# Optimization experiments

Hardware: AMD Instinct MI355X
Metric: run time of the kernel (lower is better)

Reference implementation:

```python
import jax, jax.numpy as jnp
import numpy as np

N_NODES = 100000
N_EDGES = 1600000
N_CLASS = 26
HIDDEN = 128


def gcn_conv(x, W, b, row, col, ew, n):
    """PyG GCNConv with normalize=True, add_self_loops=True (fill 1.0).

    row/col/ew already include self-loops. x: [N, Fin], W: [Fin, Fout].
    """
    deg = jax.ops.segment_sum(ew, col, num_segments=n)            # [N]
    dis = jnp.where(deg > 0, jax.lax.rsqrt(jnp.maximum(deg, 1e-30)), 0.0)
    norm = dis[row] * ew * dis[col]                               # [E+N]
    h = x @ W                                                     # [N, Fout]
    msg = h[row] * norm[:, None]                                  # gather + scale
    out = jax.ops.segment_sum(msg, col, num_segments=n)           # scatter-add
    return out + b


def setup_inputs() -> dict:
    key = jax.random.key(0)
    k1, k2, k3, k4, k5, k6, k7, k8, k9 = jax.random.split(key, 9)
    x = jax.random.normal(k1, (N_NODES, N_CLASS), dtype=jnp.float32)
    edge_index = jax.random.randint(k2, (2, N_EDGES), 0, N_NODES, dtype=jnp.int64)
    edge_weight = jax.random.uniform(k3, (N_EDGES,), dtype=jnp.float32)
    s1 = 1.0 / np.sqrt(N_CLASS)
    s2 = 1.0 / np.sqrt(HIDDEN)
    W1 = jax.random.uniform(k4, (N_CLASS, HIDDEN), jnp.float32, -s1, s1)
    b1 = jnp.zeros((HIDDEN,), jnp.float32)
    W2 = jax.random.uniform(k5, (HIDDEN, HIDDEN), jnp.float32, -s2, s2)
    b2 = jnp.zeros((HIDDEN,), jnp.float32)
    Wfc = jax.random.uniform(k6, (HIDDEN, N_CLASS), jnp.float32, -s2, s2)
    bfc = jax.random.uniform(k7, (N_CLASS,), jnp.float32, -s2, s2)
    return {"x": x, "edge_index": edge_index, "edge_weight": edge_weight,
            "W1": W1, "b1": b1, "W2": W2, "b2": b2, "Wfc": Wfc, "bfc": bfc}


def reference(x, edge_index, edge_weight, W1, b1, W2, b2, Wfc, bfc):
    n = x.shape[0]
    loop = jnp.arange(n, dtype=edge_index.dtype)
    row = jnp.concatenate([edge_index[0], loop])   # sources (with self-loops)
    col = jnp.concatenate([edge_index[1], loop])   # targets
    ew = jnp.concatenate([edge_weight, jnp.ones((n,), edge_weight.dtype)])
    h = jax.nn.relu(gcn_conv(x, W1, b1, row, col, ew, n))
    h = jax.nn.relu(gcn_conv(h, W2, b2, row, col, ew, n))
    return h @ Wfc + bfc
```

## Files before the change

### kernel.cpp

```cpp
#include <hip/hip_runtime.h>
#include <hip/hip_fp16.h>

#define N_NODES 100000
#define N_EDGES 1600000
#define HIDDEN  128
#define N_CLASS 26

#define BUK_SHIFT 9
#define BUK_DSTS  512
#define NBUK      196
#define BUK_CAP   10240
#define PB_EDGES  8192
#define PB_BLOCKS ((N_EDGES + PB_EDGES - 1) / PB_EDGES)

typedef _Float16 f16x2 __attribute__((ext_vector_type(2)));

__device__ __forceinline__ float fdot2(__half2 a, __half2 b, float c) {
#if __has_builtin(__builtin_amdgcn_fdot2)
    union { __half2 h; f16x2 v; } ua, ub;
    ua.h = a; ub.h = b;
    return __builtin_amdgcn_fdot2(ua.v, ub.v, c, false);
#else
    float2 fa = __half22float2(a), fb = __half22float2(b);
    return c + fa.x * fb.x + fa.y * fb.y;
#endif
}

union U4 { uint4 u; __half2 h[4]; };
union U2 { uint2 u; __half2 h[2]; };
union UW { int i; __half2 h; };


__global__ __launch_bounds__(1024) void bucket_kernel(const int* __restrict__ row,
                                                      const int* __restrict__ col,
                                                      const float* __restrict__ ew,
                                                      int* __restrict__ bukcnt,
                                                      int2* __restrict__ stage) {
    __shared__ int2 outst[PB_EDGES];
    __shared__ unsigned short bukof[PB_EDGES];
    __shared__ int cnt[NBUK], ofs[NBUK], cur[NBUK], gt[NBUK];
    __shared__ int sc[256];
    const int tid = threadIdx.x;
    const int e0 = blockIdx.x * PB_EDGES;
    const int nvalid = min(PB_EDGES, N_EDGES - e0);

    for (int b = tid; b < NBUK; b += 1024) { cnt[b] = 0; cur[b] = 0; }
    __syncthreads();

    int mykey[8]; float myw[8]; int mybuk[8];
#pragma unroll
    for (int i = 0; i < 8; ++i) {
        int idx = tid + i * 1024;
        mybuk[i] = -1;
        if (idx < nvalid) {
            int e = e0 + idx;
            int d = col[e], r = row[e];
            int buk = d >> BUK_SHIFT;
            mykey[i] = ((d & (BUK_DSTS - 1)) << 17) | r;
            myw[i] = ew[e];
            mybuk[i] = buk;
            atomicAdd(&cnt[buk], 1);
        }
    }
    __syncthreads();

    {
        int c = (tid < NBUK) ? cnt[tid] : 0;
        if (tid < 256) sc[tid] = c;
        __syncthreads();
        for (int o = 1; o < 256; o <<= 1) {
            int v = 0;
            if (tid < 256 && tid >= o) v = sc[tid - o];
            __syncthreads();
            if (tid < 256) sc[tid] += v;
            __syncthreads();
        }
        if (tid < NBUK) ofs[tid] = sc[tid] - c;
        __syncthreads();
    }

#pragma unroll
    for (int i = 0; i < 8; ++i) {
        if (mybuk[i] >= 0) {
            int s = ofs[mybuk[i]] + atomicAdd(&cur[mybuk[i]], 1);
            outst[s] = make_int2(mykey[i], __float_as_int(myw[i]));
            bukof[s] = (unsigned short)mybuk[i];
        }
    }
    __syncthreads();

    if (tid < NBUK) {
        int c = cnt[tid];
        int gb = (c > 0) ? atomicAdd(&bukcnt[tid], c) : 0;
        gt[tid] = tid * BUK_CAP + gb;
    }
    __syncthreads();

    for (int i = tid; i < nvalid; i += 1024) {
        int b = bukof[i];
        stage[(size_t)gt[b] + (i - ofs[b])] = outst[i];
    }
}


__global__ void bukscan_kernel(const int* __restrict__ bukcnt, int* __restrict__ bukbase,
                               int* __restrict__ start) {
    __shared__ int s[256];
    int tid = threadIdx.x;
    int c = (tid < NBUK) ? bukcnt[tid] : 0;
    s[tid] = c;
    __syncthreads();
    for (int o = 1; o < 256; o <<= 1) {
        int v = (tid >= o) ? s[tid - o] : 0;
        __syncthreads();
        s[tid] += v;
        __syncthreads();
    }
    if (tid < NBUK) bukbase[tid] = s[tid] - c;
    if (tid == 0) start[N_NODES] = N_EDGES;
}


__global__ __launch_bounds__(1024) void csr_kernel(const int2* __restrict__ stage,
                                                   const int* __restrict__ bukcnt,
                                                   const int* __restrict__ bukbase,
                                                   const float* __restrict__ x,
                                                   int* __restrict__ start,
                                                   float* __restrict__ dinv,
                                                   __half* __restrict__ x16,
                                                   int2* __restrict__ packed,
                                                   int* __restrict__ perm) {
    __shared__ unsigned int cnt5[BUK_DSTS];
    __shared__ int ofs5[BUK_DSTS];
    __shared__ unsigned int cur5[BUK_DSTS];
    __shared__ float deg5[BUK_DSTS];
    __shared__ float dv5[BUK_DSTS];
    __shared__ int sc[BUK_DSTS];
    __shared__ int dhist[128];
    __shared__ int dcur[128];
    const int tid = threadIdx.x;
    const int b = blockIdx.x;
    const int total = bukcnt[b];
    const int base = bukbase[b];
    const int2* st = stage + (size_t)b * BUK_CAP;

    for (int j = tid; j < BUK_DSTS; j += 1024) { cnt5[j] = 0; cur5[j] = 0; deg5[j] = 0.0f; }
    if (tid < 128) { dhist[tid] = 0; dcur[tid] = 0; }
    __syncthreads();

    for (int i = tid; i < total; i += 1024) {
        int2 en = st[i];
        int dl = en.x >> 17;
        atomicAdd(&cnt5[dl], 1u);
        atomicAdd(&deg5[dl], __int_as_float(en.y));
    }
    __syncthreads();

    {
        int c = (tid < BUK_DSTS) ? (int)cnt5[tid] : 0;
        if (tid < BUK_DSTS) sc[tid] = c;
        __syncthreads();
        for (int o = 1; o < BUK_DSTS; o <<= 1) {
            int v = 0;
            if (tid < BUK_DSTS && tid >= o) v = sc[tid - o];
            __syncthreads();
            if (tid < BUK_DSTS) sc[tid] += v;
            __syncthreads();
        }
        if (tid < BUK_DSTS) ofs5[tid] = sc[tid] - c;
        __syncthreads();
    }

    int myd = -1;
    {
        int d = (b << BUK_SHIFT) + tid;
        if (tid < BUK_DSTS && d < N_NODES) {
            myd = min((int)cnt5[tid], 127);
            atomicAdd(&dhist[myd], 1);
        }
    }

    if (tid < BUK_DSTS) {
        int d = (b << BUK_SHIFT) + tid;
        if (d < N_NODES) {
            float dv = rsqrtf(deg5[tid] + 1.0f);
            dv5[tid] = dv;
            dinv[d] = dv;
            start[d] = base + ofs5[tid];
        }
    }
    __syncthreads();

    if (tid < 128) sc[tid] = dhist[tid];
    __syncthreads();
    for (int o = 1; o < 128; o <<= 1) {
        int v = 0;
        if (tid < 128 && tid >= o) v = sc[tid - o];
        __syncthreads();
        if (tid < 128) sc[tid] += v;
        __syncthreads();
    }
    if (myd >= 0) {
        int rank = sc[myd] - dhist[myd] + atomicAdd(&dcur[myd], 1);
        perm[(b << BUK_SHIFT) + rank] = (b << BUK_SHIFT) + tid;
    }

    for (int t = tid; t < BUK_DSTS * 32; t += 1024) {
        int j = t >> 5, l = t & 31;
        int d = (b << BUK_SHIFT) + j;
        if (d < N_NODES) {
            float v = (l < N_CLASS) ? x[(size_t)d * N_CLASS + l] * dv5[j] : 0.0f;
            x16[((size_t)d << 5) + l] = __float2half(v);
        }
    }

    for (int i = tid; i < total; i += 1024) {
        int2 en = st[i];
        int dl = en.x >> 17;
        int src = en.x & 0x1FFFF;
        unsigned int r = atomicAdd(&cur5[dl], 1u);
        unsigned int hw = __half_as_ushort(__float2half(__int_as_float(en.y)));
        packed[(size_t)base + ofs5[dl] + (int)r] = make_int2(src, (int)(hw | (hw << 16)));
    }
}


__global__ __launch_bounds__(256) void layer1_kernel(const __half* __restrict__ x16,
                                                     const int* __restrict__ start,
                                                     const int2* __restrict__ packed,
                                                     const float* __restrict__ dinv,
                                                     const int* __restrict__ perm,
                                                     const float* __restrict__ W1,
                                                     const float* __restrict__ b1,
                                                     __half* __restrict__ h16) {
    __shared__ float axs[32][32];
    __shared__ int gl[32];
    const int tid = threadIdx.x;
    const int nb = blockIdx.x * 32;
    {
        const int j = tid >> 3;
        const int l = tid & 7;
        const int g = perm[nb + j];
        if (l == 0) gl[j] = g;
        const uint2* X = reinterpret_cast<const uint2*>(x16);
        U2 sv; sv.u = X[((size_t)g << 3) + l];
        __half2 acc0 = sv.h[0], acc1 = sv.h[1];
        int s = start[g], t = start[g + 1];
        int i = s;
        for (; i + 4 <= t; i += 4) {
            int2 p0 = packed[i], p1 = packed[i + 1], p2 = packed[i + 2], p3 = packed[i + 3];
            U2 v0, v1, v2, v3;
            v0.u = X[((size_t)p0.x << 3) + l];
            v1.u = X[((size_t)p1.x << 3) + l];
            v2.u = X[((size_t)p2.x << 3) + l];
            v3.u = X[((size_t)p3.x << 3) + l];
            UW w0, w1, w2, w3;
            w0.i = p0.y; w1.i = p1.y; w2.i = p2.y; w3.i = p3.y;
            acc0 = __hfma2(w0.h, v0.h[0], acc0); acc1 = __hfma2(w0.h, v0.h[1], acc1);
            acc0 = __hfma2(w1.h, v1.h[0], acc0); acc1 = __hfma2(w1.h, v1.h[1], acc1);
            acc0 = __hfma2(w2.h, v2.h[0], acc0); acc1 = __hfma2(w2.h, v2.h[1], acc1);
            acc0 = __hfma2(w3.h, v3.h[0], acc0); acc1 = __hfma2(w3.h, v3.h[1], acc1);
        }
        for (; i < t; ++i) {
            int2 p = packed[i];
            U2 v; v.u = X[((size_t)p.x << 3) + l];
            UW w; w.i = p.y;
            acc0 = __hfma2(w.h, v.h[0], acc0); acc1 = __hfma2(w.h, v.h[1], acc1);
        }
        float dg = dinv[g];
        float2 a = __half22float2(acc0), bb = __half22float2(acc1);
        *reinterpret_cast<float4*>(&axs[j][l * 4]) =
            make_float4(dg * a.x, dg * a.y, dg * bb.x, dg * bb.y);
    }
    __syncthreads();
    const int c = tid & 127;
    const int half = tid >> 7;
    float w[N_CLASS];
#pragma unroll
    for (int k = 0; k < N_CLASS; ++k) w[k] = W1[k * HIDDEN + c];
    const float bias = b1[c];
#pragma unroll
    for (int tt = 0; tt < 16; ++tt) {
        int n = half + 2 * tt;
        float acc = bias;
#pragma unroll
        for (int k = 0; k < N_CLASS; ++k) acc += axs[n][k] * w[k];
        h16[(size_t)gl[n] * HIDDEN + c] = __float2half(fmaxf(acc, 0.0f));
    }
}


#define CB_NODES 128
__global__ __launch_bounds__(512) void gemmC_kernel(const __half* __restrict__ h16,
                                                    const float* __restrict__ W2,
                                                    const float* __restrict__ dinv,
                                                    __half* __restrict__ p16) {
    __shared__ __half2 hs2[CB_NODES][HIDDEN / 2];
    __shared__ __half2 ws2[HIDDEN / 2][HIDDEN];
    const int tid = threadIdx.x;
    const int nb = blockIdx.x * CB_NODES;
    for (int t = tid; t < HIDDEN / 2 * HIDDEN; t += 512) {
        int k2 = t >> 7, c = t & 127;
        ws2[k2][c] = __floats2half2_rn(W2[(2 * k2) * HIDDEN + c], W2[(2 * k2 + 1) * HIDDEN + c]);
    }
    for (int t = tid; t < CB_NODES * 16; t += 512) {
        int node = nb + (t >> 4);
        reinterpret_cast<uint4*>(hs2)[t] =
            (node < N_NODES)
                ? reinterpret_cast<const uint4*>(h16)[(size_t)node * 16 + (t & 15)]
                : make_uint4(0u, 0u, 0u, 0u);
    }
    __syncthreads();
    const int c4 = (tid & 31) * 4;
    const int n0 = (tid >> 5) * 8;
    float acc[8][4] = {};
    for (int k2 = 0; k2 < HIDDEN / 2; k2 += 2) {
        U4 wa, wb;
        wa.u = *reinterpret_cast<const uint4*>(&ws2[k2][c4]);
        wb.u = *reinterpret_cast<const uint4*>(&ws2[k2 + 1][c4]);
#pragma unroll
        for (int i = 0; i < 8; ++i) {
            U2 hv; hv.u = *reinterpret_cast<const uint2*>(&hs2[n0 + i][k2]);
#pragma unroll
            for (int q = 0; q < 4; ++q) {
                acc[i][q] = fdot2(hv.h[0], wa.h[q], acc[i][q]);
                acc[i][q] = fdot2(hv.h[1], wb.h[q], acc[i][q]);
            }
        }
    }
#pragma unroll
    for (int i = 0; i < 8; ++i) {
        int node = nb + n0 + i;
        if (node < N_NODES) {
            float d = dinv[node];
            union { __half2 h2[2]; uint2 u; } pk;
            pk.h2[0] = __floats2half2_rn(d * acc[i][0], d * acc[i][1]);
            pk.h2[1] = __floats2half2_rn(d * acc[i][2], d * acc[i][3]);
            *reinterpret_cast<uint2*>(&p16[(size_t)node * HIDDEN + c4]) = pk.u;
        }
    }
}


__global__ __launch_bounds__(256) void aggfc_kernel(const __half* __restrict__ p16,
                                                    const int* __restrict__ start,
                                                    const int2* __restrict__ packed,
                                                    const float* __restrict__ dinv,
                                                    const int* __restrict__ perm,
                                                    const float* __restrict__ b2,
                                                    const float* __restrict__ Wfc,
                                                    const float* __restrict__ bfc,
                                                    float* __restrict__ out) {
    __shared__ __half2 wf2[HIDDEN / 2][N_CLASS];
    __shared__ float bfs[N_CLASS];
    __shared__ __half2 zs2[16][65];
    const int tid = threadIdx.x;
    for (int t = tid; t < HIDDEN / 2 * N_CLASS; t += 256) {
        int k2 = t / N_CLASS, j = t % N_CLASS;
        wf2[k2][j] = __floats2half2_rn(Wfc[(2 * k2) * N_CLASS + j], Wfc[(2 * k2 + 1) * N_CLASS + j]);
    }
    if (tid < N_CLASS) bfs[tid] = bfc[tid];
    __syncthreads();

    const int grp = tid >> 4;
    const int l   = tid & 15;
    const int g   = perm[blockIdx.x * 16 + grp];
    const uint4* P = reinterpret_cast<const uint4*>(p16);

    U4 sv; sv.u = P[((size_t)g << 4) + l];
    __half2 acc0 = sv.h[0], acc1 = sv.h[1], acc2 = sv.h[2], acc3 = sv.h[3];

    int s = start[g], t = start[g + 1];
    int i = s;
    for (; i + 4 <= t; i += 4) {
        int2 pa = packed[i], pb = packed[i + 1], pc = packed[i + 2], pd = packed[i + 3];
        U4 va, vb, vc, vd;
        va.u = P[((size_t)pa.x << 4) + l];
        vb.u = P[((size_t)pb.x << 4) + l];
        vc.u = P[((size_t)pc.x << 4) + l];
        vd.u = P[((size_t)pd.x << 4) + l];
        UW wa, wb, wc, wd; wa.i = pa.y; wb.i = pb.y; wc.i = pc.y; wd.i = pd.y;
        acc0 = __hfma2(wa.h, va.h[0], acc0); acc1 = __hfma2(wa.h, va.h[1], acc1);
        acc2 = __hfma2(wa.h, va.h[2], acc2); acc3 = __hfma2(wa.h, va.h[3], acc3);
        acc0 = __hfma2(wb.h, vb.h[0], acc0); acc1 = __hfma2(wb.h, vb.h[1], acc1);
        acc2 = __hfma2(wb.h, vb.h[2], acc2); acc3 = __hfma2(wb.h, vb.h[3], acc3);
        acc0 = __hfma2(wc.h, vc.h[0], acc0); acc1 = __hfma2(wc.h, vc.h[1], acc1);
        acc2 = __hfma2(wc.h, vc.h[2], acc2); acc3 = __hfma2(wc.h, vc.h[3], acc3);
        acc0 = __hfma2(wd.h, vd.h[0], acc0); acc1 = __hfma2(wd.h, vd.h[1], acc1);
        acc2 = __hfma2(wd.h, vd.h[2], acc2); acc3 = __hfma2(wd.h, vd.h[3], acc3);
    }
    for (; i < t; ++i) {
        int2 p = packed[i];
        U4 v; v.u = P[((size_t)p.x << 4) + l];
        UW w; w.i = p.y;
        acc0 = __hfma2(w.h, v.h[0], acc0); acc1 = __hfma2(w.h, v.h[1], acc1);
        acc2 = __hfma2(w.h, v.h[2], acc2); acc3 = __hfma2(w.h, v.h[3], acc3);
    }

    const float dg = dinv[g];
    const int f = l * 8;
    float4 ba = *reinterpret_cast<const float4*>(&b2[f]);
    float4 bb = *reinterpret_cast<const float4*>(&b2[f + 4]);
    float2 f0 = __half22float2(acc0), f1 = __half22float2(acc1);
    float2 f2 = __half22float2(acc2), f3 = __half22float2(acc3);
    zs2[grp][l * 4 + 0] = __floats2half2_rn(fmaxf(dg * f0.x + ba.x, 0.f), fmaxf(dg * f0.y + ba.y, 0.f));
    zs2[grp][l * 4 + 1] = __floats2half2_rn(fmaxf(dg * f1.x + ba.z, 0.f), fmaxf(dg * f1.y + ba.w, 0.f));
    zs2[grp][l * 4 + 2] = __floats2half2_rn(fmaxf(dg * f2.x + bb.x, 0.f), fmaxf(dg * f2.y + bb.y, 0.f));
    zs2[grp][l * 4 + 3] = __floats2half2_rn(fmaxf(dg * f3.x + bb.z, 0.f), fmaxf(dg * f3.y + bb.w, 0.f));
#pragma unroll
    for (int jj = l; jj < N_CLASS; jj += 16) {
        float accf = bfs[jj];
#pragma unroll 16
        for (int k2 = 0; k2 < HIDDEN / 2; ++k2)
            accf = fdot2(zs2[grp][k2], wf2[k2][jj], accf);
        out[(size_t)g * N_CLASS + jj] = accf;
    }
}


extern "C" void kernel_launch(void* const* d_in, const int* in_sizes, int n_in,
                              void* d_out, int out_size, void* d_ws, size_t ws_size,
                              hipStream_t stream) {
    const float* x   = (const float*)d_in[0];
    const int*   ei  = (const int*)  d_in[1];
    const float* ew  = (const float*)d_in[2];
    const float* W1  = (const float*)d_in[3];
    const float* b1  = (const float*)d_in[4];
    const float* W2  = (const float*)d_in[5];
    const float* b2  = (const float*)d_in[6];
    const float* Wfc = (const float*)d_in[7];
    const float* bfc = (const float*)d_in[8];
    float* out = (float*)d_out;

    const int n = N_NODES, E = N_EDGES;
    const int* row = ei;
    const int* col = ei + E;

    char* ws = (char*)d_ws;
    size_t off = 0;
    auto alloc = [&](size_t bytes) -> void* {
        void* ptr = ws + off;
        off += (bytes + 255) & ~(size_t)255;
        return ptr;
    };
    int*   bukcnt  = (int*)  alloc(NBUK * 4);
    int*   bukbase = (int*)  alloc(NBUK * 4);
    float* dinv    = (float*)alloc((size_t)n * 4);
    int*   start   = (int*)  alloc((size_t)(n + 1) * 4);
    int*   perm    = (int*)  alloc((size_t)n * 4);
    int2*  packed  = (int2*) alloc((size_t)E * 8);
    __half* x16    = (__half*)alloc((size_t)n * 32 * 2);
    __half* h16    = (__half*)alloc((size_t)n * HIDDEN * 2 < (size_t)NBUK * BUK_CAP * 8
                                        ? (size_t)NBUK * BUK_CAP * 8
                                        : (size_t)n * HIDDEN * 2);
    __half* p16    = (__half*)alloc((size_t)n * HIDDEN * 2);
    int2*  stage   = (int2*)h16;

    hipMemsetAsync(bukcnt, 0, NBUK * 4, stream);
    bucket_kernel<<<PB_BLOCKS, 1024, 0, stream>>>(row, col, ew, bukcnt, stage);
    bukscan_kernel<<<1, 256, 0, stream>>>(bukcnt, bukbase, start);
    csr_kernel<<<NBUK, 1024, 0, stream>>>(stage, bukcnt, bukbase, x, start, dinv, x16, packed, perm);

    layer1_kernel<<<(n + 31) / 32, 256, 0, stream>>>(x16, start, packed, dinv, perm, W1, b1, h16);

    gemmC_kernel<<<(n + CB_NODES - 1) / CB_NODES, 512, 0, stream>>>(h16, W2, dinv, p16);
    aggfc_kernel<<<(n + 15) / 16, 256, 0, stream>>>(p16, start, packed, dinv, perm, b2, Wfc, bfc, out);
}
```

Baseline: 221.2 us.

## Split layer-2 aggregation from final FC and deepen gather unrolling

Separates the fused aggregation+FC kernel into an aggregation kernel that writes fp16 activations to a reused buffer and a separate FC kernel. The FC kernel keeps Wfc in registers and processes 128 nodes per block, so each block no longer rebuilds the Wfc table in shared memory and the gather kernel drops its shared-memory use, which should raise occupancy. The edge-gather loops in layer 1 and layer 2 are also unrolled to 8 loads in flight to hide memory latency. The trade-off is an extra kernel launch and an extra write and read of a 100000x128 fp16 intermediate, plus higher register pressure in the unrolled loops.

```diff
diff --git a/kernel.cpp b/kernel.cpp
--- a/kernel.cpp
+++ b/kernel.cpp
@@ -247,19 +247,18 @@
         __half2 acc0 = sv.h[0], acc1 = sv.h[1];
         int s = start[g], t = start[g + 1];
         int i = s;
-        for (; i + 4 <= t; i += 4) {
-            int2 p0 = packed[i], p1 = packed[i + 1], p2 = packed[i + 2], p3 = packed[i + 3];
-            U2 v0, v1, v2, v3;
-            v0.u = X[((size_t)p0.x << 3) + l];
-            v1.u = X[((size_t)p1.x << 3) + l];
-            v2.u = X[((size_t)p2.x << 3) + l];
-            v3.u = X[((size_t)p3.x << 3) + l];
-            UW w0, w1, w2, w3;
-            w0.i = p0.y; w1.i = p1.y; w2.i = p2.y; w3.i = p3.y;
-            acc0 = __hfma2(w0.h, v0.h[0], acc0); acc1 = __hfma2(w0.h, v0.h[1], acc1);
-            acc0 = __hfma2(w1.h, v1.h[0], acc0); acc1 = __hfma2(w1.h, v1.h[1], acc1);
-            acc0 = __hfma2(w2.h, v2.h[0], acc0); acc1 = __hfma2(w2.h, v2.h[1], acc1);
-            acc0 = __hfma2(w3.h, v3.h[0], acc0); acc1 = __hfma2(w3.h, v3.h[1], acc1);
+        for (; i + 8 <= t; i += 8) {
+            int2 pk[8]; U2 vv[8];
+#pragma unroll
+            for (int u = 0; u < 8; ++u) pk[u] = packed[i + u];
+#pragma unroll
+            for (int u = 0; u < 8; ++u) vv[u].u = X[((size_t)pk[u].x << 3) + l];
+#pragma unroll
+            for (int u = 0; u < 8; ++u) {
+                UW w; w.i = pk[u].y;
+                acc0 = __hfma2(w.h, vv[u].h[0], acc0);
+                acc1 = __hfma2(w.h, vv[u].h[1], acc1);
+            }
         }
         for (; i < t; ++i) {
             int2 p = packed[i];
@@ -342,28 +341,15 @@
 }
 
 
-__global__ __launch_bounds__(256) void aggfc_kernel(const __half* __restrict__ p16,
-                                                    const int* __restrict__ start,
-                                                    const int2* __restrict__ packed,
-                                                    const float* __restrict__ dinv,
-                                                    const int* __restrict__ perm,
-                                                    const float* __restrict__ b2,
-                                                    const float* __restrict__ Wfc,
-                                                    const float* __restrict__ bfc,
-                                                    float* __restrict__ out) {
-    __shared__ __half2 wf2[HIDDEN / 2][N_CLASS];
-    __shared__ float bfs[N_CLASS];
-    __shared__ __half2 zs2[16][65];
-    const int tid = threadIdx.x;
-    for (int t = tid; t < HIDDEN / 2 * N_CLASS; t += 256) {
-        int k2 = t / N_CLASS, j = t % N_CLASS;
-        wf2[k2][j] = __floats2half2_rn(Wfc[(2 * k2) * N_CLASS + j], Wfc[(2 * k2 + 1) * N_CLASS + j]);
-    }
-    if (tid < N_CLASS) bfs[tid] = bfc[tid];
-    __syncthreads();
-
-    const int grp = tid >> 4;
-    const int l   = tid & 15;
+__global__ __launch_bounds__(256) void agg2_kernel(const __half* __restrict__ p16,
+                                                   const int* __restrict__ start,
+                                                   const int2* __restrict__ packed,
+                                                   const float* __restrict__ dinv,
+                                                   const int* __restrict__ perm,
+                                                   const float* __restrict__ b2,
+                                                   __half* __restrict__ z16) {
+    const int grp = threadIdx.x >> 4;
+    const int l   = threadIdx.x & 15;
     const int g   = perm[blockIdx.x * 16 + grp];
     const uint4* P = reinterpret_cast<const uint4*>(p16);
 
@@ -372,22 +358,35 @@
 
     int s = start[g], t = start[g + 1];
     int i = s;
+    for (; i + 8 <= t; i += 8) {
+        int2 pk[8]; U4 vv[8];
+#pragma unroll
+        for (int u = 0; u < 8; ++u) pk[u] = packed[i + u];
+#pragma unroll
+        for (int u = 0; u < 8; ++u) vv[u].u = P[((size_t)pk[u].x << 4) + l];
+#pragma unroll
+        for (int u = 0; u < 8; ++u) {
+            UW w; w.i = pk[u].y;
+            acc0 = __hfma2(w.h, vv[u].h[0], acc0);
+            acc1 = __hfma2(w.h, vv[u].h[1], acc1);
+            acc2 = __hfma2(w.h, vv[u].h[2], acc2);
+            acc3 = __hfma2(w.h, vv[u].h[3], acc3);
+        }
+    }
     for (; i + 4 <= t; i += 4) {
-        int2 pa = packed[i], pb = packed[i + 1], pc = packed[i + 2], pd = packed[i + 3];
-        U4 va, vb, vc, vd;
-        va.u = P[((size_t)pa.x << 4) + l];
-        vb.u = P[((size_t)pb.x << 4) + l];
-        vc.u = P[((size_t)pc.x << 4) + l];
-        vd.u = P[((size_t)pd.x << 4) + l];
-        UW wa, wb, wc, wd; wa.i = pa.y; wb.i = pb.y; wc.i = pc.y; wd.i = pd.y;
-        acc0 = __hfma2(wa.h, va.h[0], acc0); acc1 = __hfma2(wa.h, va.h[1], acc1);
-        acc2 = __hfma2(wa.h, va.h[2], acc2); acc3 = __hfma2(wa.h, va.h[3], acc3);
-        acc0 = __hfma2(wb.h, vb.h[0], acc0); acc1 = __hfma2(wb.h, vb.h[1], acc1);
-        acc2 = __hfma2(wb.h, vb.h[2], acc2); acc3 = __hfma2(wb.h, vb.h[3], acc3);
-        acc0 = __hfma2(wc.h, vc.h[0], acc0); acc1 = __hfma2(wc.h, vc.h[1], acc1);
-        acc2 = __hfma2(wc.h, vc.h[2], acc2); acc3 = __hfma2(wc.h, vc.h[3], acc3);
-        acc0 = __hfma2(wd.h, vd.h[0], acc0); acc1 = __hfma2(wd.h, vd.h[1], acc1);
-        acc2 = __hfma2(wd.h, vd.h[2], acc2); acc3 = __hfma2(wd.h, vd.h[3], acc3);
+        int2 pk[4]; U4 vv[4];
+#pragma unroll
+        for (int u = 0; u < 4; ++u) pk[u] = packed[i + u];
+#pragma unroll
+        for (int u = 0; u < 4; ++u) vv[u].u = P[((size_t)pk[u].x << 4) + l];
+#pragma unroll
+        for (int u = 0; u < 4; ++u) {
+            UW w; w.i = pk[u].y;
+            acc0 = __hfma2(w.h, vv[u].h[0], acc0);
+            acc1 = __hfma2(w.h, vv[u].h[1], acc1);
+            acc2 = __hfma2(w.h, vv[u].h[2], acc2);
+            acc3 = __hfma2(w.h, vv[u].h[3], acc3);
+        }
     }
     for (; i < t; ++i) {
         int2 p = packed[i];
@@ -403,17 +402,53 @@
     float4 bb = *reinterpret_cast<const float4*>(&b2[f + 4]);
     float2 f0 = __half22float2(acc0), f1 = __half22float2(acc1);
     float2 f2 = __half22float2(acc2), f3 = __half22float2(acc3);
-    zs2[grp][l * 4 + 0] = __floats2half2_rn(fmaxf(dg * f0.x + ba.x, 0.f), fmaxf(dg * f0.y + ba.y, 0.f));
-    zs2[grp][l * 4 + 1] = __floats2half2_rn(fmaxf(dg * f1.x + ba.z, 0.f), fmaxf(dg * f1.y + ba.w, 0.f));
-    zs2[grp][l * 4 + 2] = __floats2half2_rn(fmaxf(dg * f2.x + bb.x, 0.f), fmaxf(dg * f2.y + bb.y, 0.f));
-    zs2[grp][l * 4 + 3] = __floats2half2_rn(fmaxf(dg * f3.x + bb.z, 0.f), fmaxf(dg * f3.y + bb.w, 0.f));
-#pragma unroll
-    for (int jj = l; jj < N_CLASS; jj += 16) {
-        float accf = bfs[jj];
-#pragma unroll 16
+    U4 zz;
+    zz.h[0] = __floats2half2_rn(fmaxf(dg * f0.x + ba.x, 0.f), fmaxf(dg * f0.y + ba.y, 0.f));
+    zz.h[1] = __floats2half2_rn(fmaxf(dg * f1.x + ba.z, 0.f), fmaxf(dg * f1.y + ba.w, 0.f));
+    zz.h[2] = __floats2half2_rn(fmaxf(dg * f2.x + bb.x, 0.f), fmaxf(dg * f2.y + bb.y, 0.f));
+    zz.h[3] = __floats2half2_rn(fmaxf(dg * f3.x + bb.z, 0.f), fmaxf(dg * f3.y + bb.w, 0.f));
+    reinterpret_cast<uint4*>(z16)[((size_t)g << 4) + l] = zz.u;
+}
+
+
+#define FC_NODES 128
+__global__ __launch_bounds__(256) void fc_kernel(const __half* __restrict__ z16,
+                                                 const float* __restrict__ Wfc,
+                                                 const float* __restrict__ bfc,
+                                                 float* __restrict__ out) {
+    __shared__ __align__(16) __half2 zsh[FC_NODES][68];
+    const int tid = threadIdx.x;
+    const int nb = blockIdx.x * FC_NODES;
+    for (int t = tid; t < FC_NODES * 16; t += 256) {
+        int n = t >> 4, q = t & 15;
+        int node = nb + n;
+        uint4 v = (node < N_NODES)
+                      ? reinterpret_cast<const uint4*>(z16)[(size_t)node * 16 + q]
+                      : make_uint4(0u, 0u, 0u, 0u);
+        *reinterpret_cast<uint4*>(&zsh[n][q * 4]) = v;
+    }
+    const int j = tid & 31;
+    const int slice = tid >> 5;
+    __half2 wreg[HIDDEN / 2];
+    float bj = 0.0f;
+    if (j < N_CLASS) {
+        bj = bfc[j];
+#pragma unroll
         for (int k2 = 0; k2 < HIDDEN / 2; ++k2)
-            accf = fdot2(zs2[grp][k2], wf2[k2][jj], accf);
-        out[(size_t)g * N_CLASS + jj] = accf;
+            wreg[k2] = __floats2half2_rn(Wfc[(2 * k2) * N_CLASS + j],
+                                         Wfc[(2 * k2 + 1) * N_CLASS + j]);
+    }
+    __syncthreads();
+    if (j >= N_CLASS) return;
+    for (int n = slice; n < FC_NODES; n += 8) {
+        int node = nb + n;
+        if (node < N_NODES) {
+            float acc = bj;
+#pragma unroll
+            for (int k2 = 0; k2 < HIDDEN / 2; ++k2)
+                acc = fdot2(zsh[n][k2], wreg[k2], acc);
+            out[(size_t)node * N_CLASS + j] = acc;
+        }
     }
 }
 
@@ -455,6 +490,7 @@
                                         : (size_t)n * HIDDEN * 2);
     __half* p16    = (__half*)alloc((size_t)n * HIDDEN * 2);
     int2*  stage   = (int2*)h16;
+    __half* z16    = h16;
 
     hipMemsetAsync(bukcnt, 0, NBUK * 4, stream);
     bucket_kernel<<<PB_BLOCKS, 1024, 0, stream>>>(row, col, ew, bukcnt, stage);
@@ -464,5 +500,7 @@
     layer1_kernel<<<(n + 31) / 32, 256, 0, stream>>>(x16, start, packed, dinv, perm, W1, b1, h16);
 
     gemmC_kernel<<<(n + CB_NODES - 1) / CB_NODES, 512, 0, stream>>>(h16, W2, dinv, p16);
-    aggfc_kernel<<<(n + 15) / 16, 256, 0, stream>>>(p16, start, packed, dinv, perm, b2, Wfc, bfc, out);
-}
+    agg2_kernel<<<(n + 15) / 16, 256, 0, stream>>>(p16, start, packed, dinv, perm, b2, z16);
+
+    fc_kernel<<<(n + FC_NODES - 1) / FC_NODES, 256, 0, stream>>>(z16, Wfc, bfc, out);
+}
```

Measured after the change: 237.0 us. 7.2% more time.
